# Kernel tuning notes

Measured on AMD Instinct MI355X. Metric: run time of the kernel, lower is better.

## Reference

```python
import jax, jax.numpy as jnp
import numpy as np

B, S, E = 2, 2048, 1024
H = 16
D = E // H          # head dim = 64
K_TOP = 64          # top-k tokens kept per query in sparse branch
M = 256             # performer kernel feature dim
EPS = 1e-6


def setup_inputs() -> dict:
    key = jax.random.key(0)
    ks = jax.random.split(key, 16)
    sc = 0.02
    p = {
        'x': jax.random.normal(ks[0], (B, S, E), jnp.float32),
        # sparse-attention branch params
        'Wq_s': jax.random.normal(ks[1], (E, E), jnp.float32) * sc,
        'Wk_s': jax.random.normal(ks[2], (E, E), jnp.float32) * sc,
        'Wv_s': jax.random.normal(ks[3], (E, E), jnp.float32) * sc,
        'Wo_s': jax.random.normal(ks[4], (E, E), jnp.float32) * sc,
        'bq_s': jnp.zeros((E,), jnp.float32),
        'bk_s': jnp.zeros((E,), jnp.float32),
        'bv_s': jnp.zeros((E,), jnp.float32),
        'bo_s': jnp.zeros((E,), jnp.float32),
        # performer branch params
        'Wq_p': jax.random.normal(ks[5], (E, E), jnp.float32) * sc,
        'Wk_p': jax.random.normal(ks[6], (E, E), jnp.float32) * sc,
        'Wv_p': jax.random.normal(ks[7], (E, E), jnp.float32) * sc,
        'Wo_p': jax.random.normal(ks[8], (E, E), jnp.float32) * sc,
        'bo_p': jnp.zeros((E,), jnp.float32),
        'Wfeat': jax.random.normal(ks[9], (D, M), jnp.float32) / np.sqrt(D),
        # gate
        'Wg': jax.random.normal(ks[10], (E, 2), jnp.float32) * sc,
        'bg': jnp.zeros((2,), jnp.float32),
    }
    return p


def _split_heads(t):
    # [B,S,E] -> [B,H,S,D]
    return t.reshape(B, S, H, D).transpose(0, 2, 1, 3)


def _merge_heads(t):
    # [B,H,S,D] -> [B,S,E]
    return t.transpose(0, 2, 1, 3).reshape(B, S, E)


def _sparse_attn(x, Wq, bq, Wk, bk, Wv, bv, Wo, bo):
    q = _split_heads(x @ Wq + bq)
    k = _split_heads(x @ Wk + bk)
    v = _split_heads(x @ Wv + bv)
    scores = jnp.einsum('bhqd,bhkd->bhqk', q, k) / np.sqrt(D)  # [B,H,S,S]
    # keep only top-K scores per query row
    topv = jax.lax.top_k(scores, K_TOP)[0]
    thresh = topv[..., -1:]
    neg = jnp.finfo(scores.dtype).min
    masked = jnp.where(scores >= thresh, scores, neg)
    attn = jax.nn.softmax(masked, axis=-1)
    out = jnp.einsum('bhqk,bhkd->bhqd', attn, v)
    return _merge_heads(out) @ Wo + bo


def _performer_attn(x, Wq, Wk, Wv, Wo, bo, Wfeat):
    q = _split_heads(x @ Wq)
    k = _split_heads(x @ Wk)
    v = _split_heads(x @ Wv)
    # learned relu feature map (FAVOR-style linear attention)
    phi_q = jax.nn.relu(jnp.einsum('bhsd,dm->bhsm', q, Wfeat)) + EPS
    phi_k = jax.nn.relu(jnp.einsum('bhsd,dm->bhsm', k, Wfeat)) + EPS
    kv = jnp.einsum('bhsm,bhsd->bhmd', phi_k, v)      # [B,H,M,D]
    z = phi_k.sum(axis=2)                              # [B,H,M]
    num = jnp.einsum('bhsm,bhmd->bhsd', phi_q, kv)
    den = jnp.einsum('bhsm,bhm->bhs', phi_q, z)[..., None] + EPS
    return _merge_heads(num / den) @ Wo + bo


def reference(x, Wq_s, Wk_s, Wv_s, Wo_s, bq_s, bk_s, bv_s, bo_s,
              Wq_p, Wk_p, Wv_p, Wo_p, bo_p, Wfeat, Wg, bg):
    sparse_out = _sparse_attn(x, Wq_s, bq_s, Wk_s, bk_s, Wv_s, bv_s, Wo_s, bo_s)
    perf_out = _performer_attn(x, Wq_p, Wk_p, Wv_p, Wo_p, bo_p, Wfeat)
    avg_hidden = x.mean(axis=1)                        # [B,E]
    gate = jax.nn.softmax(avg_hidden @ Wg + bg, axis=-1)  # [B,2]
    w_s = gate[:, 0][:, None, None]
    w_p = gate[:, 1][:, None, None]
    # dropout is identity in eval/reference mode
    return w_s * sparse_out + w_p * perf_out
```

## Files before the change

### kernel.cpp

```cpp
#include <hip/hip_runtime.h>


constexpr int cB = 2, cS = 2048, cE = 1024, cH = 16, cD = 64, cKTOP = 64, cM = 256;
constexpr float cEPS = 1e-6f;

typedef _Float16 half8 __attribute__((ext_vector_type(8)));
typedef float f32x16 __attribute__((ext_vector_type(16)));

__device__ __forceinline__ unsigned int f2key(float f) {
    unsigned int u = __float_as_uint(f);
    return (u & 0x80000000u) ? ~u : (u | 0x80000000u);
}

__device__ __forceinline__ unsigned short h2u(_Float16 h) {
    union { _Float16 h; unsigned short u; } x; x.h = h; return x.u;
}

__device__ __forceinline__ half8 ld_half8(const unsigned short* p) {
    union { uint4 u; half8 h; } x;
    x.u = *(const uint4*)p;
    return x.h;
}

__global__ __launch_bounds__(256)
void gemm_qk_blas(const float* __restrict__ A,
                  const float* __restrict__ W,
                  const float* __restrict__ bias,
                  float* __restrict__ C, int K, int N)
{
    __shared__ __align__(16) float As[16][68];
    __shared__ __align__(16) float Bs[16][68];
    const int t  = threadIdx.x;
    const int r0 = blockIdx.y * 64;
    const int c0 = blockIdx.x * 64;
    const int tm = t >> 4, tn = t & 15;
    float pacc[4][4] = {};
    float cacc[4][4] = {};

    const int ar = t >> 2, ak = (t & 3) * 4;
    const int bk = t >> 4, bc = (t & 15) * 4;

    for (int k0 = 0; k0 < K; k0 += 16) {
        const float4 av = *(const float4*)(A + (size_t)(r0 + ar) * K + (k0 + ak));
        const float4 bv = *(const float4*)(W + (size_t)(k0 + bk) * N + (c0 + bc));
        As[ak + 0][ar] = av.x;
        As[ak + 1][ar] = av.y;
        As[ak + 2][ar] = av.z;
        As[ak + 3][ar] = av.w;
        *(float4*)&Bs[bk][bc] = bv;
        __syncthreads();
        #pragma unroll
        for (int kk = 0; kk < 16; ++kk) {
            const float4 a4 = *(const float4*)&As[kk][tm * 4];
            const float4 b4 = *(const float4*)&Bs[kk][tn * 4];
            const float a[4]  = {a4.x, a4.y, a4.z, a4.w};
            const float bb[4] = {b4.x, b4.y, b4.z, b4.w};
            #pragma unroll
            for (int i = 0; i < 4; ++i)
                #pragma unroll
                for (int j = 0; j < 4; ++j)
                    pacc[i][j] = fmaf(a[i], bb[j], pacc[i][j]);
        }
        __syncthreads();
        const int kn = k0 + 16;
        if (kn == 384 || kn == 768 || kn == K) {
            #pragma unroll
            for (int i = 0; i < 4; ++i)
                #pragma unroll
                for (int j = 0; j < 4; ++j) {
                    cacc[i][j] = cacc[i][j] + pacc[i][j];
                    pacc[i][j] = 0.f;
                }
        }
    }
    #pragma unroll
    for (int i = 0; i < 4; ++i) {
        const int r = r0 + tm * 4 + i;
        const int c = c0 + tn * 4;
        float4 v;
        v.x = cacc[i][0] + bias[c + 0];
        v.y = cacc[i][1] + bias[c + 1];
        v.z = cacc[i][2] + bias[c + 2];
        v.w = cacc[i][3] + bias[c + 3];
        *(float4*)&C[(size_t)r * N + c] = v;
    }
}

__global__ __launch_bounds__(256)
void conv_wT(const float* __restrict__ W,
             unsigned short* __restrict__ wthi,
             unsigned short* __restrict__ wtlo)
{
    __shared__ float tile[64][68];
    const int t  = threadIdx.x;
    const int k0 = blockIdx.y * 64;
    const int n0 = blockIdx.x * 64;
    const int r  = t >> 4, c4 = (t & 15) * 4;
    #pragma unroll
    for (int i = 0; i < 4; ++i) {
        const int k = r + 16 * i;
        const float4 v = *(const float4*)&W[(size_t)(k0 + k) * cE + n0 + c4];
        tile[k][c4 + 0] = v.x; tile[k][c4 + 1] = v.y;
        tile[k][c4 + 2] = v.z; tile[k][c4 + 3] = v.w;
    }
    __syncthreads();
    #pragma unroll
    for (int i = 0; i < 4; ++i) {
        const int n = r + 16 * i;
        unsigned int hp[2], lp[2];
        #pragma unroll
        for (int p = 0; p < 2; ++p) {
            unsigned short hh[2], ll[2];
            #pragma unroll
            for (int j = 0; j < 2; ++j) {
                const float f = tile[c4 + p * 2 + j][n];
                const _Float16 h = (_Float16)f;
                hh[j] = h2u(h);
                ll[j] = h2u((_Float16)(f - (float)h));
            }
            hp[p] = (unsigned int)hh[0] | ((unsigned int)hh[1] << 16);
            lp[p] = (unsigned int)ll[0] | ((unsigned int)ll[1] << 16);
        }
        uint2 hv, lv;
        hv.x = hp[0]; hv.y = hp[1];
        lv.x = lp[0]; lv.y = lp[1];
        *(uint2*)&wthi[(size_t)(n0 + n) * cE + k0 + c4] = hv;
        *(uint2*)&wtlo[(size_t)(n0 + n) * cE + k0 + c4] = lv;
    }
}

__global__ __launch_bounds__(256)
void gemm_hilo(const float* __restrict__ A,
               const unsigned short* __restrict__ wthi,
               const unsigned short* __restrict__ wtlo,
               const float* __restrict__ bias,
               float* __restrict__ C)
{
    __shared__ __align__(16) unsigned short Ah[128][24];
    __shared__ __align__(16) unsigned short Al[128][24];
    __shared__ __align__(16) unsigned short Bh[64][24];
    __shared__ __align__(16) unsigned short Bl[64][24];

    const int t    = threadIdx.x;
    const int lane = t & 63, wave = t >> 6;
    const int wr   = wave >> 1, wc = wave & 1;
    const int r0   = blockIdx.y * 128, c0 = blockIdx.x * 64;
    const int fr   = lane & 31, g5 = lane >> 5;

    const int arow = t >> 1, aka = (t & 1) * 8;
    const int bsel = t >> 7;
    const int brow = (t & 127) >> 1, bkb = (t & 1) * 8;
    const unsigned short* wsrc = bsel ? wtlo : wthi;

    f32x16 acc0 = {0.f,0.f,0.f,0.f,0.f,0.f,0.f,0.f,0.f,0.f,0.f,0.f,0.f,0.f,0.f,0.f};
    f32x16 acc1 = {0.f,0.f,0.f,0.f,0.f,0.f,0.f,0.f,0.f,0.f,0.f,0.f,0.f,0.f,0.f,0.f};

    for (int k0 = 0; k0 < cE; k0 += 16) {
        const float4 x0 = *(const float4*)&A[(size_t)(r0 + arow) * cE + k0 + aka];
        const float4 x1 = *(const float4*)&A[(size_t)(r0 + arow) * cE + k0 + aka + 4];
        const float xf[8] = {x0.x, x0.y, x0.z, x0.w, x1.x, x1.y, x1.z, x1.w};
        unsigned int hw[4], lw[4];
        #pragma unroll
        for (int p = 0; p < 4; ++p) {
            unsigned short hh[2], ll[2];
            #pragma unroll
            for (int j = 0; j < 2; ++j) {
                const float f = xf[p * 2 + j];
                const _Float16 h = (_Float16)f;
                hh[j] = h2u(h);
                ll[j] = h2u((_Float16)(f - (float)h));
            }
            hw[p] = (unsigned int)hh[0] | ((unsigned int)hh[1] << 16);
            lw[p] = (unsigned int)ll[0] | ((unsigned int)ll[1] << 16);
        }
        uint4 hv, lv;
        hv.x = hw[0]; hv.y = hw[1]; hv.z = hw[2]; hv.w = hw[3];
        lv.x = lw[0]; lv.y = lw[1]; lv.z = lw[2]; lv.w = lw[3];
        *(uint4*)&Ah[arow][aka] = hv;
        *(uint4*)&Al[arow][aka] = lv;

        const uint4 wv = *(const uint4*)&wsrc[(size_t)(c0 + brow) * cE + k0 + bkb];
        if (bsel) *(uint4*)&Bl[brow][bkb] = wv;
        else      *(uint4*)&Bh[brow][bkb] = wv;
        __syncthreads();

        const half8 a0h = ld_half8(&Ah[wr * 64 + fr][g5 * 8]);
        const half8 a0l = ld_half8(&Al[wr * 64 + fr][g5 * 8]);
        const half8 a1h = ld_half8(&Ah[wr * 64 + 32 + fr][g5 * 8]);
        const half8 a1l = ld_half8(&Al[wr * 64 + 32 + fr][g5 * 8]);
        const half8 bh  = ld_half8(&Bh[wc * 32 + fr][g5 * 8]);
        const half8 bl  = ld_half8(&Bl[wc * 32 + fr][g5 * 8]);

        acc0 = __builtin_amdgcn_mfma_f32_32x32x16_f16(a0l, bh, acc0, 0, 0, 0);
        acc0 = __builtin_amdgcn_mfma_f32_32x32x16_f16(a0h, bl, acc0, 0, 0, 0);
        acc0 = __builtin_amdgcn_mfma_f32_32x32x16_f16(a0h, bh, acc0, 0, 0, 0);
        acc1 = __builtin_amdgcn_mfma_f32_32x32x16_f16(a1l, bh, acc1, 0, 0, 0);
        acc1 = __builtin_amdgcn_mfma_f32_32x32x16_f16(a1h, bl, acc1, 0, 0, 0);
        acc1 = __builtin_amdgcn_mfma_f32_32x32x16_f16(a1h, bh, acc1, 0, 0, 0);
        __syncthreads();
    }

    const int col = c0 + wc * 32 + fr;
    const float bv = bias ? bias[col] : 0.f;
    #pragma unroll
    for (int rg = 0; rg < 16; ++rg) {
        const int row = r0 + wr * 64 + (rg & 3) + 8 * (rg >> 2) + 4 * g5;
        C[(size_t)row * cE + col] = acc0[rg] + bv;
    }
    #pragma unroll
    for (int rg = 0; rg < 16; ++rg) {
        const int row = r0 + wr * 64 + 32 + (rg & 3) + 8 * (rg >> 2) + 4 * g5;
        C[(size_t)row * cE + col] = acc1[rg] + bv;
    }
}

__global__ __launch_bounds__(256)
void out_gemm_hilo(const float* __restrict__ As_, const float* __restrict__ Ap_,
                   const unsigned short* __restrict__ w1hi,
                   const unsigned short* __restrict__ w1lo,
                   const unsigned short* __restrict__ w2hi,
                   const unsigned short* __restrict__ w2lo,
                   const float* __restrict__ bos, const float* __restrict__ bop,
                   const float* __restrict__ gates, float* __restrict__ out)
{
    __shared__ __align__(16) unsigned short A1h[128][24], A1l[128][24];
    __shared__ __align__(16) unsigned short A2h[128][24], A2l[128][24];
    __shared__ __align__(16) unsigned short B1h[64][24],  B1l[64][24];
    __shared__ __align__(16) unsigned short B2h[64][24],  B2l[64][24];

    const int t    = threadIdx.x;
    const int lane = t & 63, wave = t >> 6;
    const int wr   = wave >> 1, wc = wave & 1;
    const int r0   = blockIdx.y * 128, c0 = blockIdx.x * 64;
    const int fr   = lane & 31, g5 = lane >> 5;
    const int b    = r0 >> 11;
    const float gs = gates[b * 2 + 0], gp = gates[b * 2 + 1];

    const int arow = t >> 1, aka = (t & 1) * 8;
    const int bsel = t >> 7;
    const int brow = (t & 127) >> 1, bkb = (t & 1) * 8;
    const unsigned short* s1 = bsel ? w1lo : w1hi;
    const unsigned short* s2 = bsel ? w2lo : w2hi;

    f32x16 acc0 = {0.f,0.f,0.f,0.f,0.f,0.f,0.f,0.f,0.f,0.f,0.f,0.f,0.f,0.f,0.f,0.f};
    f32x16 acc1 = {0.f,0.f,0.f,0.f,0.f,0.f,0.f,0.f,0.f,0.f,0.f,0.f,0.f,0.f,0.f,0.f};

    for (int k0 = 0; k0 < cE; k0 += 16) {
        {
            const float4 x0 = *(const float4*)&As_[(size_t)(r0 + arow) * cE + k0 + aka];
            const float4 x1 = *(const float4*)&As_[(size_t)(r0 + arow) * cE + k0 + aka + 4];
            const float xf[8] = {x0.x * gs, x0.y * gs, x0.z * gs, x0.w * gs,
                                 x1.x * gs, x1.y * gs, x1.z * gs, x1.w * gs};
            unsigned int hw[4], lw[4];
            #pragma unroll
            for (int p = 0; p < 4; ++p) {
                unsigned short hh[2], ll[2];
                #pragma unroll
                for (int j = 0; j < 2; ++j) {
                    const float f = xf[p * 2 + j];
                    const _Float16 h = (_Float16)f;
                    hh[j] = h2u(h);
                    ll[j] = h2u((_Float16)(f - (float)h));
                }
                hw[p] = (unsigned int)hh[0] | ((unsigned int)hh[1] << 16);
                lw[p] = (unsigned int)ll[0] | ((unsigned int)ll[1] << 16);
            }
            uint4 hv, lv;
            hv.x = hw[0]; hv.y = hw[1]; hv.z = hw[2]; hv.w = hw[3];
            lv.x = lw[0]; lv.y = lw[1]; lv.z = lw[2]; lv.w = lw[3];
            *(uint4*)&A1h[arow][aka] = hv;
            *(uint4*)&A1l[arow][aka] = lv;
        }
        {
            const float4 x0 = *(const float4*)&Ap_[(size_t)(r0 + arow) * cE + k0 + aka];
            const float4 x1 = *(const float4*)&Ap_[(size_t)(r0 + arow) * cE + k0 + aka + 4];
            const float xf[8] = {x0.x * gp, x0.y * gp, x0.z * gp, x0.w * gp,
                                 x1.x * gp, x1.y * gp, x1.z * gp, x1.w * gp};
            unsigned int hw[4], lw[4];
            #pragma unroll
            for (int p = 0; p < 4; ++p) {
                unsigned short hh[2], ll[2];
                #pragma unroll
                for (int j = 0; j < 2; ++j) {
                    const float f = xf[p * 2 + j];
                    const _Float16 h = (_Float16)f;
                    hh[j] = h2u(h);
                    ll[j] = h2u((_Float16)(f - (float)h));
                }
                hw[p] = (unsigned int)hh[0] | ((unsigned int)hh[1] << 16);
                lw[p] = (unsigned int)ll[0] | ((unsigned int)ll[1] << 16);
            }
            uint4 hv, lv;
            hv.x = hw[0]; hv.y = hw[1]; hv.z = hw[2]; hv.w = hw[3];
            lv.x = lw[0]; lv.y = lw[1]; lv.z = lw[2]; lv.w = lw[3];
            *(uint4*)&A2h[arow][aka] = hv;
            *(uint4*)&A2l[arow][aka] = lv;
        }
        {
            const uint4 w1 = *(const uint4*)&s1[(size_t)(c0 + brow) * cE + k0 + bkb];
            if (bsel) *(uint4*)&B1l[brow][bkb] = w1;
            else      *(uint4*)&B1h[brow][bkb] = w1;
            const uint4 w2 = *(const uint4*)&s2[(size_t)(c0 + brow) * cE + k0 + bkb];
            if (bsel) *(uint4*)&B2l[brow][bkb] = w2;
            else      *(uint4*)&B2h[brow][bkb] = w2;
        }
        __syncthreads();

        const half8 b1h = ld_half8(&B1h[wc * 32 + fr][g5 * 8]);
        const half8 b1l = ld_half8(&B1l[wc * 32 + fr][g5 * 8]);
        const half8 b2h = ld_half8(&B2h[wc * 32 + fr][g5 * 8]);
        const half8 b2l = ld_half8(&B2l[wc * 32 + fr][g5 * 8]);
        {
            const half8 a1h = ld_half8(&A1h[wr * 64 + fr][g5 * 8]);
            const half8 a1l = ld_half8(&A1l[wr * 64 + fr][g5 * 8]);
            const half8 a2h = ld_half8(&A2h[wr * 64 + fr][g5 * 8]);
            const half8 a2l = ld_half8(&A2l[wr * 64 + fr][g5 * 8]);
            acc0 = __builtin_amdgcn_mfma_f32_32x32x16_f16(a1l, b1h, acc0, 0, 0, 0);
            acc0 = __builtin_amdgcn_mfma_f32_32x32x16_f16(a1h, b1l, acc0, 0, 0, 0);
            acc0 = __builtin_amdgcn_mfma_f32_32x32x16_f16(a1h, b1h, acc0, 0, 0, 0);
            acc0 = __builtin_amdgcn_mfma_f32_32x32x16_f16(a2l, b2h, acc0, 0, 0, 0);
            acc0 = __builtin_amdgcn_mfma_f32_32x32x16_f16(a2h, b2l, acc0, 0, 0, 0);
            acc0 = __builtin_amdgcn_mfma_f32_32x32x16_f16(a2h, b2h, acc0, 0, 0, 0);
        }
        {
            const half8 a1h = ld_half8(&A1h[wr * 64 + 32 + fr][g5 * 8]);
            const half8 a1l = ld_half8(&A1l[wr * 64 + 32 + fr][g5 * 8]);
            const half8 a2h = ld_half8(&A2h[wr * 64 + 32 + fr][g5 * 8]);
            const half8 a2l = ld_half8(&A2l[wr * 64 + 32 + fr][g5 * 8]);
            acc1 = __builtin_amdgcn_mfma_f32_32x32x16_f16(a1l, b1h, acc1, 0, 0, 0);
            acc1 = __builtin_amdgcn_mfma_f32_32x32x16_f16(a1h, b1l, acc1, 0, 0, 0);
            acc1 = __builtin_amdgcn_mfma_f32_32x32x16_f16(a1h, b1h, acc1, 0, 0, 0);
            acc1 = __builtin_amdgcn_mfma_f32_32x32x16_f16(a2l, b2h, acc1, 0, 0, 0);
            acc1 = __builtin_amdgcn_mfma_f32_32x32x16_f16(a2h, b2l, acc1, 0, 0, 0);
            acc1 = __builtin_amdgcn_mfma_f32_32x32x16_f16(a2h, b2h, acc1, 0, 0, 0);
        }
        __syncthreads();
    }

    const int col = c0 + wc * 32 + fr;
    const float bv = gs * bos[col] + gp * bop[col];
    #pragma unroll
    for (int rg = 0; rg < 16; ++rg) {
        const int row = r0 + wr * 64 + (rg & 3) + 8 * (rg >> 2) + 4 * g5;
        out[(size_t)row * cE + col] = acc0[rg] + bv;
    }
    #pragma unroll
    for (int rg = 0; rg < 16; ++rg) {
        const int row = r0 + wr * 64 + 32 + (rg & 3) + 8 * (rg >> 2) + 4 * g5;
        out[(size_t)row * cE + col] = acc1[rg] + bv;
    }
}

__global__ __launch_bounds__(256)
void transpose_k(const float* __restrict__ Ks, float* __restrict__ KsT)
{
    __shared__ float tile[64][65];
    const int t  = threadIdx.x;
    const int bh = blockIdx.y;
    const int b  = bh >> 4;
    const int h64 = (bh & 15) * 64;
    const int s0 = blockIdx.x * 64;
    const int sr = t >> 4;
    const int d4 = (t & 15) * 4;
    #pragma unroll
    for (int i = 0; i < 4; ++i) {
        const int s = sr + 16 * i;
        float4 v = *(const float4*)&Ks[((size_t)(b * cS + s0 + s)) * cE + h64 + d4];
        tile[s][d4 + 0] = v.x; tile[s][d4 + 1] = v.y;
        tile[s][d4 + 2] = v.z; tile[s][d4 + 3] = v.w;
    }
    __syncthreads();
    const int s4 = (t & 15) * 4;
    #pragma unroll
    for (int i = 0; i < 4; ++i) {
        const int d = (t >> 4) + 16 * i;
        float4 w;
        w.x = tile[s4 + 0][d]; w.y = tile[s4 + 1][d];
        w.z = tile[s4 + 2][d]; w.w = tile[s4 + 3][d];
        *(float4*)&KsT[((size_t)(bh * 64 + d)) * cS + s0 + s4] = w;
    }
}

__global__ __launch_bounds__(256, 4)
void sparse_attn(const float* __restrict__ Q, const float* __restrict__ KT,
                 const float* __restrict__ Ks, const float* __restrict__ V,
                 float* __restrict__ O)
{
    __shared__ float QfT[64][8];
    __shared__ unsigned int hist[8][257];
    __shared__ unsigned int hist2[8][257];
    __shared__ unsigned short cidx[8][128];
    __shared__ double cval[8][128];
    __shared__ float cw[8][128];
    __shared__ int cnt[8];
    __shared__ int t16hi[8], rem[8], t16[8];
    __shared__ double T64s[8], s65s[8], rowm[8];

    const int t   = threadIdx.x;
    const int bh  = blockIdx.y;
    const int b   = bh >> 4;
    const int h64 = (bh & 15) * 64;
    const int q0  = blockIdx.x * 8;

    if (t < 128) {
        const int r = t >> 4, c4 = (t & 15) * 4;
        const float4 v =
            *(const float4*)&Q[((size_t)(b * cS + q0 + r)) * cE + h64 + c4];
        QfT[c4 + 0][r] = v.x; QfT[c4 + 1][r] = v.y;
        QfT[c4 + 2][r] = v.z; QfT[c4 + 3][r] = v.w;
    }
    for (int i = t; i < 8 * 257; i += 256) {
        (&hist[0][0])[i]  = 0u;
        (&hist2[0][0])[i] = 0u;
    }
    if (t < 8) cnt[t] = 0;
    __syncthreads();

    const float* KTh = KT + (size_t)bh * 64 * cS;
    float4 acc[2][8];
    #pragma unroll
    for (int j = 0; j < 2; ++j)
        #pragma unroll
        for (int r = 0; r < 8; ++r) acc[j][r] = make_float4(0.f, 0.f, 0.f, 0.f);

    #pragma unroll 4
    for (int d = 0; d < 64; ++d) {
        const float4 k0 = *(const float4*)&KTh[(size_t)d * cS + 4 * t];
        const float4 k1 = *(const float4*)&KTh[(size_t)d * cS + 1024 + 4 * t];
        const float4 qa = *(const float4*)&QfT[d][0];
        const float4 qb = *(const float4*)&QfT[d][4];
        const float qr[8] = {qa.x, qa.y, qa.z, qa.w, qb.x, qb.y, qb.z, qb.w};
        #pragma unroll
        for (int r = 0; r < 8; ++r) {
            acc[0][r].x = fmaf(qr[r], k0.x, acc[0][r].x);
            acc[0][r].y = fmaf(qr[r], k0.y, acc[0][r].y);
            acc[0][r].z = fmaf(qr[r], k0.z, acc[0][r].z);
            acc[0][r].w = fmaf(qr[r], k0.w, acc[0][r].w);
            acc[1][r].x = fmaf(qr[r], k1.x, acc[1][r].x);
            acc[1][r].y = fmaf(qr[r], k1.y, acc[1][r].y);
            acc[1][r].z = fmaf(qr[r], k1.z, acc[1][r].z);
            acc[1][r].w = fmaf(qr[r], k1.w, acc[1][r].w);
        }
    }
    unsigned int su[2][8][2];
    #pragma unroll
    for (int j = 0; j < 2; ++j)
        #pragma unroll
        for (int r = 0; r < 8; ++r) {
            su[j][r][0] = (f2key(acc[j][r].x * 0.125f) >> 16)
                        | ((f2key(acc[j][r].y * 0.125f) >> 16) << 16);
            su[j][r][1] = (f2key(acc[j][r].z * 0.125f) >> 16)
                        | ((f2key(acc[j][r].w * 0.125f) >> 16) << 16);
        }

    #pragma unroll
    for (int j = 0; j < 2; ++j)
        #pragma unroll
        for (int r = 0; r < 8; ++r)
            #pragma unroll
            for (int w = 0; w < 2; ++w) {
                const unsigned int u = su[j][r][w];
                atomicAdd(&hist[r][(u & 0xFFFFu) >> 8], 1u);
                atomicAdd(&hist[r][u >> 24], 1u);
            }
    __syncthreads();
    if (t < 8) {
        int need = cKTOP + 1;
        int hb = 0;
        for (int bin = 255; bin >= 0; --bin) {
            const int c = (int)hist[t][bin];
            if (c >= need) { hb = bin; break; }
            need -= c;
        }
        t16hi[t] = hb;
        rem[t] = need;
    }
    __syncthreads();
    #pragma unroll
    for (int j = 0; j < 2; ++j)
        #pragma unroll
        for (int r = 0; r < 8; ++r) {
            const unsigned int hb = (unsigned int)t16hi[r];
            #pragma unroll
            for (int w = 0; w < 2; ++w) {
                const unsigned int u  = su[j][r][w];
                const unsigned int lo = u & 0xFFFFu;
                const unsigned int hi = u >> 16;
                if ((lo >> 8) == hb) atomicAdd(&hist2[r][lo & 255u], 1u);
                if ((hi >> 8) == hb) atomicAdd(&hist2[r][hi & 255u], 1u);
            }
        }
    __syncthreads();
    if (t < 8) {
        int need = rem[t];
        int lb = 0;
        for (int bin = 255; bin >= 0; --bin) {
            const int c = (int)hist2[t][bin];
            if (c >= need) { lb = bin; break; }
            need -= c;
        }
        t16[t] = (t16hi[t] << 8) | lb;
    }
    __syncthreads();

    #pragma unroll
    for (int j = 0; j < 2; ++j)
        #pragma unroll
        for (int r = 0; r < 8; ++r) {
            const int thr16 = max(t16[r] - 2, 0);
            #pragma unroll
            for (int w = 0; w < 2; ++w) {
                const unsigned int u = su[j][r][w];
                const int v0 = (int)(u & 0xFFFFu);
                const int v1 = (int)(u >> 16);
                if (v0 >= thr16) {
                    const int slot = atomicAdd(&cnt[r], 1);
                    if (slot < 128)
                        cidx[r][slot] = (unsigned short)(j * 1024 + 4 * t + w * 2);
                }
                if (v1 >= thr16) {
                    const int slot = atomicAdd(&cnt[r], 1);
                    if (slot < 128)
                        cidx[r][slot] = (unsigned short)(j * 1024 + 4 * t + w * 2 + 1);
                }
            }
        }
    __syncthreads();

    const int wv = t >> 6, lane = t & 63;
    #pragma unroll
    for (int rx = 0; rx < 2; ++rx) {
        const int rr = wv * 2 + rx;
        const int n = min(cnt[rr], 128);
        for (int c = lane; c < n; c += 64) {
            const int key = cidx[rr][c];
            const float* kp = Ks + ((size_t)(b * cS + key)) * cE + h64;
            double a = 0.0;
            #pragma unroll 4
            for (int d4 = 0; d4 < 64; d4 += 4) {
                const float4 kv = *(const float4*)&kp[d4];
                a = fma((double)QfT[d4 + 0][rr], (double)kv.x, a);
                a = fma((double)QfT[d4 + 1][rr], (double)kv.y, a);
                a = fma((double)QfT[d4 + 2][rr], (double)kv.z, a);
                a = fma((double)QfT[d4 + 3][rr], (double)kv.w, a);
            }
            cval[rr][c] = a * 0.125;
        }
    }
    __syncthreads();

    #pragma unroll
    for (int rx = 0; rx < 2; ++rx) {
        const int rr = wv * 2 + rx;
        const int n = min(cnt[rr], 128);
        for (int c = lane; c < n; c += 64) {
            const double v = cval[rr][c];
            int rank = 0;
            for (int i = 0; i < n; ++i) rank += (cval[rr][i] > v) ? 1 : 0;
            if (rank == 0)  rowm[rr] = v;
            if (rank == 63) T64s[rr] = v;
            if (rank == 64) s65s[rr] = v;
        }
    }
    __syncthreads();

    #pragma unroll
    for (int rx = 0; rx < 2; ++rx) {
        const int rr = wv * 2 + rx;
        const int n = min(cnt[rr], 128);
        const double T64 = T64s[rr], s65 = s65s[rr], m = rowm[rr];
        float za = 0.f;
        for (int c = lane; c < n; c += 64) {
            const double v = cval[rr][c];
            if (v >= T64) za += expf((float)(v - m));
        }
        #pragma unroll
        for (int off = 32; off >= 1; off >>= 1)
            za += __shfl_xor(za, off);
        const float g   = (float)(T64 - s65);
        const float gm  = fmaxf(g - 5e-7f, 0.f);
        const float wB  = 0.5f * erfcf(gm * (1.0f / 2.2e-6f));
        const float wA  = 1.f - wB;
        const float e64 = expf((float)(T64 - m));
        const float e65 = expf((float)(s65 - m));
        const float ZB  = za - e64 + e65;
        const float cIn = wA / za + wB / ZB;
        const float c64 = wA / za;
        const float c65 = wB / ZB;
        for (int c = lane; c < n; c += 64) {
            const double v = cval[rr][c];
            float cc = 0.f;
            if (v > T64)       cc = cIn;
            else if (v == T64) cc = c64;
            else if (v == s65) cc = c65;
            cw[rr][c] = (cc != 0.f) ? cc * expf((float)(v - m)) : 0.f;
        }
    }
    __syncthreads();

    #pragma unroll
    for (int rx = 0; rx < 2; ++rx) {
        const int rr = wv * 2 + rx;
        const int n = min(cnt[rr], 128);
        float o = 0.f;
        int j = 0;
        for (; j + 8 <= n; j += 8) {
            float wreg[8];
            int   kreg[8];
            #pragma unroll
            for (int u = 0; u < 8; ++u) {
                wreg[u] = cw[rr][j + u];
                kreg[u] = cidx[rr][j + u];
            }
            float vreg[8];
            #pragma unroll
            for (int u = 0; u < 8; ++u)
                vreg[u] = V[((size_t)(b * cS + kreg[u])) * cE + h64 + lane];
            #pragma unroll
            for (int u = 0; u < 8; ++u)
                o = fmaf(wreg[u], vreg[u], o);
        }
        for (; j < n; ++j)
            o = fmaf(cw[rr][j],
                     V[((size_t)(b * cS + cidx[rr][j])) * cE + h64 + lane], o);
        O[((size_t)(b * cS + q0 + rr)) * cE + h64 + lane] = o;
    }
}

__global__ __launch_bounds__(256)
void perf_kv(const float* __restrict__ Kp, const float* __restrict__ Vp,
             const float* __restrict__ Wfeat,
             float* __restrict__ kvpart, float* __restrict__ zpart)
{
    __shared__ __align__(16) float Wf[64][68];
    __shared__ __align__(16) float Kt[64][68];
    __shared__ __align__(16) float Vt[64][68];
    __shared__ __align__(16) float Ph[64][68];
    const int t    = threadIdx.x;
    const int mc   = blockIdx.x & 3;
    const int sc   = blockIdx.x >> 2;
    const int bh   = blockIdx.y;
    const int b    = bh >> 4;
    const int h64  = (bh & 15) * 64;
    const int m0   = mc * 64;
    const int sbase = sc * 1024;

    #pragma unroll
    for (int i = 0; i < 4; ++i) {
        const int lin = t + 256 * i;
        const int d   = lin >> 4;
        const int m4  = (lin & 15) * 4;
        *(float4*)&Wf[d][m4] = *(const float4*)&Wfeat[d * cM + m0 + m4];
    }

    const int tm = t >> 4, tn = t & 15;
    const int sr = tm * 4;
    const int cn = tn * 4;
    float akv[4][4] = {};
    float az = 0.f;

    for (int st = 0; st < 16; ++st) {
        const int s0g = sbase + st * 64;
        __syncthreads();
        #pragma unroll
        for (int i = 0; i < 4; ++i) {
            const int row = tm + 16 * i;
            const size_t base = ((size_t)(b * cS + s0g + row)) * cE + h64 + cn;
            *(float4*)&Kt[row][cn] = *(const float4*)&Kp[base];
            *(float4*)&Vt[row][cn] = *(const float4*)&Vp[base];
        }
        __syncthreads();
        float4 p0 = {0,0,0,0}, p1 = {0,0,0,0}, p2 = {0,0,0,0}, p3 = {0,0,0,0};
        #pragma unroll 8
        for (int d = 0; d < 64; ++d) {
            const float4 wv = *(const float4*)&Wf[d][cn];
            const float k0 = Kt[sr + 0][d], k1 = Kt[sr + 1][d];
            const float k2 = Kt[sr + 2][d], k3 = Kt[sr + 3][d];
            p0.x = fmaf(k0, wv.x, p0.x); p0.y = fmaf(k0, wv.y, p0.y);
            p0.z = fmaf(k0, wv.z, p0.z); p0.w = fmaf(k0, wv.w, p0.w);
            p1.x = fmaf(k1, wv.x, p1.x); p1.y = fmaf(k1, wv.y, p1.y);
            p1.z = fmaf(k1, wv.z, p1.z); p1.w = fmaf(k1, wv.w, p1.w);
            p2.x = fmaf(k2, wv.x, p2.x); p2.y = fmaf(k2, wv.y, p2.y);
// ... 96 lines not shown
        if (t < 64)
            zl[t] = zpart[(size_t)bh * cM + m0 + t] + zpart[(size_t)(32 + bh) * cM + m0 + t];
        __syncthreads();
        float4 p0 = {0,0,0,0}, p1 = {0,0,0,0}, p2 = {0,0,0,0}, p3 = {0,0,0,0};
        #pragma unroll 8
        for (int d = 0; d < 64; ++d) {
            const float4 wv = *(const float4*)&Wf[d][cn];
            const float q0 = Qt[sr + 0][d], q1 = Qt[sr + 1][d];
            const float q2 = Qt[sr + 2][d], q3 = Qt[sr + 3][d];
            p0.x = fmaf(q0, wv.x, p0.x); p0.y = fmaf(q0, wv.y, p0.y);
            p0.z = fmaf(q0, wv.z, p0.z); p0.w = fmaf(q0, wv.w, p0.w);
            p1.x = fmaf(q1, wv.x, p1.x); p1.y = fmaf(q1, wv.y, p1.y);
            p1.z = fmaf(q1, wv.z, p1.z); p1.w = fmaf(q1, wv.w, p1.w);
            p2.x = fmaf(q2, wv.x, p2.x); p2.y = fmaf(q2, wv.y, p2.y);
            p2.z = fmaf(q2, wv.z, p2.z); p2.w = fmaf(q2, wv.w, p2.w);
            p3.x = fmaf(q3, wv.x, p3.x); p3.y = fmaf(q3, wv.y, p3.y);
            p3.z = fmaf(q3, wv.z, p3.z); p3.w = fmaf(q3, wv.w, p3.w);
        }
        p0.x = fmaxf(p0.x, 0.f) + cEPS; p0.y = fmaxf(p0.y, 0.f) + cEPS;
        p0.z = fmaxf(p0.z, 0.f) + cEPS; p0.w = fmaxf(p0.w, 0.f) + cEPS;
        p1.x = fmaxf(p1.x, 0.f) + cEPS; p1.y = fmaxf(p1.y, 0.f) + cEPS;
        p1.z = fmaxf(p1.z, 0.f) + cEPS; p1.w = fmaxf(p1.w, 0.f) + cEPS;
        p2.x = fmaxf(p2.x, 0.f) + cEPS; p2.y = fmaxf(p2.y, 0.f) + cEPS;
        p2.z = fmaxf(p2.z, 0.f) + cEPS; p2.w = fmaxf(p2.w, 0.f) + cEPS;
        p3.x = fmaxf(p3.x, 0.f) + cEPS; p3.y = fmaxf(p3.y, 0.f) + cEPS;
        p3.z = fmaxf(p3.z, 0.f) + cEPS; p3.w = fmaxf(p3.w, 0.f) + cEPS;
        *(float4*)&Ph[sr + 0][cn] = p0;
        *(float4*)&Ph[sr + 1][cn] = p1;
        *(float4*)&Ph[sr + 2][cn] = p2;
        *(float4*)&Ph[sr + 3][cn] = p3;
        __syncthreads();
        #pragma unroll 8
        for (int mm = 0; mm < 64; ++mm) {
            const float4 kvv = *(const float4*)&KV[mm][cn];
            const float a0 = Ph[sr + 0][mm], a1 = Ph[sr + 1][mm];
            const float a2 = Ph[sr + 2][mm], a3 = Ph[sr + 3][mm];
            num[0][0] = fmaf(a0, kvv.x, num[0][0]); num[0][1] = fmaf(a0, kvv.y, num[0][1]);
            num[0][2] = fmaf(a0, kvv.z, num[0][2]); num[0][3] = fmaf(a0, kvv.w, num[0][3]);
            num[1][0] = fmaf(a1, kvv.x, num[1][0]); num[1][1] = fmaf(a1, kvv.y, num[1][1]);
            num[1][2] = fmaf(a1, kvv.z, num[1][2]); num[1][3] = fmaf(a1, kvv.w, num[1][3]);
            num[2][0] = fmaf(a2, kvv.x, num[2][0]); num[2][1] = fmaf(a2, kvv.y, num[2][1]);
            num[2][2] = fmaf(a2, kvv.z, num[2][2]); num[2][3] = fmaf(a2, kvv.w, num[2][3]);
            num[3][0] = fmaf(a3, kvv.x, num[3][0]); num[3][1] = fmaf(a3, kvv.y, num[3][1]);
            num[3][2] = fmaf(a3, kvv.z, num[3][2]); num[3][3] = fmaf(a3, kvv.w, num[3][3]);
        }
        if (t < 64) {
            float a = 0.f;
            #pragma unroll
            for (int m4 = 0; m4 < 64; m4 += 4) {
                const float4 ph = *(const float4*)&Ph[t][m4];
                const float4 zz = *(const float4*)&zl[m4];
                a = fmaf(ph.x, zz.x, a); a = fmaf(ph.y, zz.y, a);
                a = fmaf(ph.z, zz.z, a); a = fmaf(ph.w, zz.w, a);
            }
            dacc += a;
        }
    }
    __syncthreads();
    if (t < 64) den[t] = dacc + cEPS;
    __syncthreads();
    #pragma unroll
    for (int i = 0; i < 4; ++i) {
        const float di = 1.f / den[sr + i];
        float4 v;
        v.x = num[i][0] * di; v.y = num[i][1] * di;
        v.z = num[i][2] * di; v.w = num[i][3] * di;
        *(float4*)&Ap[((size_t)(b * cS + s0 + sr + i)) * cE + h64 + cn] = v;
    }
}

__global__ __launch_bounds__(256)
void gate_avg(const float* __restrict__ x, double* __restrict__ avgpart)
{
    const int i  = blockIdx.x * 256 + threadIdx.x;
    const int sc = blockIdx.y;
    const int b  = i >> 10, e = i & 1023;
    double acc = 0.0;
    const int sEnd = sc * 128 + 128;
    for (int s = sc * 128; s < sEnd; ++s)
        acc += (double)x[((size_t)(b * cS + s)) * cE + e];
    avgpart[(size_t)sc * 2048 + i] = acc;
}

__global__ void gate_final(const double* __restrict__ avgpart, const float* __restrict__ Wg,
                           const float* __restrict__ bg, float* __restrict__ gates)
{
    const int t = threadIdx.x;
    const int b = t >> 6, lane = t & 63;
    float l0 = 0.f, l1 = 0.f;
    for (int e = lane; e < cE; e += 64) {
        double s = 0.0;
        #pragma unroll
        for (int sc = 0; sc < 16; ++sc)
            s += avgpart[(size_t)sc * 2048 + b * 1024 + e];
        const float a = (float)(s / (double)cS);
        l0 = fmaf(a, Wg[e * 2 + 0], l0);
        l1 = fmaf(a, Wg[e * 2 + 1], l1);
    }
    for (int off = 32; off >= 1; off >>= 1) {
        l0 += __shfl_down(l0, off);
        l1 += __shfl_down(l1, off);
    }
    if (lane == 0) {
        l0 += bg[0]; l1 += bg[1];
        const float m = fmaxf(l0, l1);
        const float e0 = expf(l0 - m), e1 = expf(l1 - m);
        const float s = e0 + e1;
        gates[b * 2 + 0] = e0 / s;
        gates[b * 2 + 1] = e1 / s;
    }
}

extern "C" void kernel_launch(void* const* d_in, const int* in_sizes, int n_in,
                              void* d_out, int out_size, void* d_ws, size_t ws_size,
                              hipStream_t stream)
{
    (void)in_sizes; (void)n_in; (void)out_size; (void)ws_size;
    const float* x     = (const float*)d_in[0];
    const float* Wq_s  = (const float*)d_in[1];
    const float* Wk_s  = (const float*)d_in[2];
    const float* Wv_s  = (const float*)d_in[3];
    const float* Wo_s  = (const float*)d_in[4];
    const float* bq_s  = (const float*)d_in[5];
    const float* bk_s  = (const float*)d_in[6];
    const float* bv_s  = (const float*)d_in[7];
    const float* bo_s  = (const float*)d_in[8];
    const float* Wq_p  = (const float*)d_in[9];
    const float* Wk_p  = (const float*)d_in[10];
    const float* Wv_p  = (const float*)d_in[11];
    const float* Wo_p  = (const float*)d_in[12];
    const float* bo_p  = (const float*)d_in[13];
    const float* Wfeat = (const float*)d_in[14];
    const float* Wg    = (const float*)d_in[15];
    const float* bg    = (const float*)d_in[16];

    float* ws = (float*)d_ws;
    const size_t NRE = (size_t)cB * cS * cE;
    float* Qs    = ws;
    float* Ks    = Qs + NRE;
    float* KsT   = Ks + NRE;
    float* Vs    = KsT + NRE;
    float* Asout = Vs + NRE;
    float* kvpart = Asout + NRE;
    float* zpart  = kvpart + (size_t)2 * 32 * cM * cD;
    double* avgpart = (double*)(zpart + (size_t)2 * 32 * cM);
    float* gates = (float*)(avgpart + (size_t)16 * 2048);
    unsigned short* wthi  = (unsigned short*)(gates + 16);
    unsigned short* wtlo  = wthi + (size_t)cE * cE;
    unsigned short* wo1hi = wtlo + (size_t)cE * cE;
    unsigned short* wo1lo = wo1hi + (size_t)cE * cE;
    unsigned short* wo2hi = wo1lo + (size_t)cE * cE;
    unsigned short* wo2lo = wo2hi + (size_t)cE * cE;

    conv_wT<<<dim3(16, 16), 256, 0, stream>>>(Wo_s, wo1hi, wo1lo);
    conv_wT<<<dim3(16, 16), 256, 0, stream>>>(Wo_p, wo2hi, wo2lo);

    gemm_qk_blas<<<dim3(16, 64), 256, 0, stream>>>(x, Wq_s, bq_s, Qs, cE, cE);
    gemm_qk_blas<<<dim3(16, 64), 256, 0, stream>>>(x, Wk_s, bk_s, Ks, cE, cE);
    conv_wT<<<dim3(16, 16), 256, 0, stream>>>(Wv_s, wthi, wtlo);
    gemm_hilo<<<dim3(16, 32), 256, 0, stream>>>(x, wthi, wtlo, bv_s, Vs);
    transpose_k<<<dim3(32, 32), 256, 0, stream>>>(Ks, KsT);
    sparse_attn<<<dim3(256, 32), 256, 0, stream>>>(Qs, KsT, Ks, Vs, Asout);

    float* Qp    = Qs;
    float* Kp    = Ks;
    float* Vp    = Vs;
    float* Apout = KsT;
    conv_wT<<<dim3(16, 16), 256, 0, stream>>>(Wq_p, wthi, wtlo);
    gemm_hilo<<<dim3(16, 32), 256, 0, stream>>>(x, wthi, wtlo, nullptr, Qp);
    conv_wT<<<dim3(16, 16), 256, 0, stream>>>(Wk_p, wthi, wtlo);
    gemm_hilo<<<dim3(16, 32), 256, 0, stream>>>(x, wthi, wtlo, nullptr, Kp);
    conv_wT<<<dim3(16, 16), 256, 0, stream>>>(Wv_p, wthi, wtlo);
    gemm_hilo<<<dim3(16, 32), 256, 0, stream>>>(x, wthi, wtlo, nullptr, Vp);
    perf_kv<<<dim3(8, 32), 256, 0, stream>>>(Kp, Vp, Wfeat, kvpart, zpart);
    perf_numden<<<dim3(32, 32), 256, 0, stream>>>(Qp, Wfeat, kvpart, zpart, Apout);

    gate_avg<<<dim3(8, 16), 256, 0, stream>>>(x, avgpart);
    gate_final<<<dim3(1), 128, 0, stream>>>(avgpart, Wg, bg, gates);
    out_gemm_hilo<<<dim3(16, 32), 256, 0, stream>>>(Asout, Apout,
                                                    wo1hi, wo1lo, wo2hi, wo2lo,
                                                    bo_s, bo_p, gates,
                                                    (float*)d_out);
}
```

Before: 1.572 ms.

## Replace atomic radix-histogram threshold search with wave-reduced binary search

Finds the per-row 16-bit top-k threshold key with a 16-step binary search instead of two 256-bin LDS histograms built with atomics. Each step counts elements at or above the midpoint per thread, reduces the counts with wave shuffles, and combines the four wave partials through a small double-buffered shared array. This removes the histogram zeroing, the contended LDS atomics and the serial single-thread bin scans. In exchange it adds 16 block barriers and 16×8 shuffle reductions per block.

```diff
diff --git a/kernel.cpp b/kernel.cpp
--- a/kernel.cpp
+++ b/kernel.cpp
@@ -387,13 +387,11 @@
                  float* __restrict__ O)
 {
     __shared__ float QfT[64][8];
-    __shared__ unsigned int hist[8][257];
-    __shared__ unsigned int hist2[8][257];
+    __shared__ int wcnt[2][4][8];
     __shared__ unsigned short cidx[8][128];
     __shared__ double cval[8][128];
     __shared__ float cw[8][128];
     __shared__ int cnt[8];
-    __shared__ int t16hi[8], rem[8], t16[8];
     __shared__ double T64s[8], s65s[8], rowm[8];
 
     const int t   = threadIdx.x;
@@ -409,12 +407,10 @@
         QfT[c4 + 0][r] = v.x; QfT[c4 + 1][r] = v.y;
         QfT[c4 + 2][r] = v.z; QfT[c4 + 3][r] = v.w;
     }
-    for (int i = t; i < 8 * 257; i += 256) {
-        (&hist[0][0])[i]  = 0u;
-        (&hist2[0][0])[i] = 0u;
-    }
     if (t < 8) cnt[t] = 0;
     __syncthreads();
+
+    const int wv = t >> 6, lane = t & 63;
 
     const float* KTh = KT + (size_t)bh * 64 * cS;
     float4 acc[2][8];
@@ -453,61 +449,43 @@
                         | ((f2key(acc[j][r].w * 0.125f) >> 16) << 16);
         }
 
+    int lo[8], hi[8];
+    #pragma unroll
+    for (int r = 0; r < 8; ++r) { lo[r] = 0; hi[r] = 65536; }
+
+    for (int it = 0; it < 16; ++it) {
+        #pragma unroll
+        for (int r = 0; r < 8; ++r) {
+            const int mid = (lo[r] + hi[r]) >> 1;
+            int c = 0;
+            #pragma unroll
+            for (int j = 0; j < 2; ++j)
+                #pragma unroll
+                for (int w = 0; w < 2; ++w) {
+                    const unsigned int u = su[j][r][w];
+                    c += ((int)(u & 0xFFFFu) >= mid) ? 1 : 0;
+                    c += ((int)(u >> 16)     >= mid) ? 1 : 0;
+                }
+            #pragma unroll
+            for (int off = 32; off >= 1; off >>= 1)
+                c += __shfl_xor(c, off);
+            if (lane == 0) wcnt[it & 1][wv][r] = c;
+        }
+        __syncthreads();
+        #pragma unroll
+        for (int r = 0; r < 8; ++r) {
+            const int mid = (lo[r] + hi[r]) >> 1;
+            const int tot = wcnt[it & 1][0][r] + wcnt[it & 1][1][r]
+                          + wcnt[it & 1][2][r] + wcnt[it & 1][3][r];
+            if (tot >= cKTOP + 1) lo[r] = mid; else hi[r] = mid;
+        }
+    }
+
     #pragma unroll
     for (int j = 0; j < 2; ++j)
         #pragma unroll
-        for (int r = 0; r < 8; ++r)
-            #pragma unroll
-            for (int w = 0; w < 2; ++w) {
-                const unsigned int u = su[j][r][w];
-                atomicAdd(&hist[r][(u & 0xFFFFu) >> 8], 1u);
-                atomicAdd(&hist[r][u >> 24], 1u);
-            }
-    __syncthreads();
-    if (t < 8) {
-        int need = cKTOP + 1;
-        int hb = 0;
-        for (int bin = 255; bin >= 0; --bin) {
-            const int c = (int)hist[t][bin];
-            if (c >= need) { hb = bin; break; }
-            need -= c;
-        }
-        t16hi[t] = hb;
-        rem[t] = need;
-    }
-    __syncthreads();
-    #pragma unroll
-    for (int j = 0; j < 2; ++j)
-        #pragma unroll
         for (int r = 0; r < 8; ++r) {
-            const unsigned int hb = (unsigned int)t16hi[r];
-            #pragma unroll
-            for (int w = 0; w < 2; ++w) {
-                const unsigned int u  = su[j][r][w];
-                const unsigned int lo = u & 0xFFFFu;
-                const unsigned int hi = u >> 16;
-                if ((lo >> 8) == hb) atomicAdd(&hist2[r][lo & 255u], 1u);
-                if ((hi >> 8) == hb) atomicAdd(&hist2[r][hi & 255u], 1u);
-            }
-        }
-    __syncthreads();
-    if (t < 8) {
-        int need = rem[t];
-        int lb = 0;
-        for (int bin = 255; bin >= 0; --bin) {
-            const int c = (int)hist2[t][bin];
-            if (c >= need) { lb = bin; break; }
-            need -= c;
-        }
-        t16[t] = (t16hi[t] << 8) | lb;
-    }
-    __syncthreads();
-
-    #pragma unroll
-    for (int j = 0; j < 2; ++j)
-        #pragma unroll
-        for (int r = 0; r < 8; ++r) {
-            const int thr16 = max(t16[r] - 2, 0);
+            const int thr16 = max(lo[r] - 2, 0);
             #pragma unroll
             for (int w = 0; w < 2; ++w) {
                 const unsigned int u = su[j][r][w];
@@ -527,7 +505,6 @@
         }
     __syncthreads();
 
-    const int wv = t >> 6, lane = t & 63;
     #pragma unroll
     for (int rx = 0; rx < 2; ++rx) {
         const int rr = wv * 2 + rx;
```

Measured after the change: 1.606 ms. 2.2% more time.

## Use fp16 MFMA for sparse top-k candidate scoring and drop K transpose

Applied to the files above, without the earlier changes.

The K projection GEMM now also writes an fp16 copy of K, and the sparse attention kernel computes the approximate score matrix with 32x32x16 fp16 MFMA instructions instead of fp32 FMAs over a transposed K. This removes the transpose_k kernel and the fp32 scalar score loop, and reuses one histogram buffer for both radix passes to cut shared memory. The candidate threshold margin is widened from 2 to 3 bins to absorb fp16 rounding error. Exact scores are still recomputed in double for the selected candidates, but the lower precision risks missing a true top-k key or overflowing the 128-slot candidate buffer.

```diff
diff --git a/kernel.cpp b/kernel.cpp
--- a/kernel.cpp
+++ b/kernel.cpp
@@ -26,7 +26,9 @@
 void gemm_qk_blas(const float* __restrict__ A,
                   const float* __restrict__ W,
                   const float* __restrict__ bias,
-                  float* __restrict__ C, int K, int N)
+                  float* __restrict__ C,
+                  unsigned short* __restrict__ khi,
+                  int K, int N)
 {
     __shared__ __align__(16) float As[16][68];
     __shared__ __align__(16) float Bs[16][68];
@@ -83,6 +85,14 @@
         v.z = cacc[i][2] + bias[c + 2];
         v.w = cacc[i][3] + bias[c + 3];
         *(float4*)&C[(size_t)r * N + c] = v;
+        if (khi) {
+            ushort4 hs;
+            hs.x = h2u((_Float16)v.x);
+            hs.y = h2u((_Float16)v.y);
+            hs.z = h2u((_Float16)v.z);
+            hs.w = h2u((_Float16)v.w);
+            *(ushort4*)&khi[(size_t)r * N + c] = hs;
+        }
     }
 }
 
@@ -351,44 +361,15 @@
     }
 }
 
-__global__ __launch_bounds__(256)
-void transpose_k(const float* __restrict__ Ks, float* __restrict__ KsT)
-{
-    __shared__ float tile[64][65];
-    const int t  = threadIdx.x;
-    const int bh = blockIdx.y;
-    const int b  = bh >> 4;
-    const int h64 = (bh & 15) * 64;
-    const int s0 = blockIdx.x * 64;
-    const int sr = t >> 4;
-    const int d4 = (t & 15) * 4;
-    #pragma unroll
-    for (int i = 0; i < 4; ++i) {
-        const int s = sr + 16 * i;
-        float4 v = *(const float4*)&Ks[((size_t)(b * cS + s0 + s)) * cE + h64 + d4];
-        tile[s][d4 + 0] = v.x; tile[s][d4 + 1] = v.y;
-        tile[s][d4 + 2] = v.z; tile[s][d4 + 3] = v.w;
-    }
-    __syncthreads();
-    const int s4 = (t & 15) * 4;
-    #pragma unroll
-    for (int i = 0; i < 4; ++i) {
-        const int d = (t >> 4) + 16 * i;
-        float4 w;
-        w.x = tile[s4 + 0][d]; w.y = tile[s4 + 1][d];
-        w.z = tile[s4 + 2][d]; w.w = tile[s4 + 3][d];
-        *(float4*)&KsT[((size_t)(bh * 64 + d)) * cS + s0 + s4] = w;
-    }
-}
-
 __global__ __launch_bounds__(256, 4)
-void sparse_attn(const float* __restrict__ Q, const float* __restrict__ KT,
+void sparse_attn(const float* __restrict__ Q,
+                 const unsigned short* __restrict__ Khi,
                  const float* __restrict__ Ks, const float* __restrict__ V,
                  float* __restrict__ O)
 {
     __shared__ float QfT[64][8];
+    __shared__ __align__(16) unsigned short Qhi[8][72];
     __shared__ unsigned int hist[8][257];
-    __shared__ unsigned int hist2[8][257];
     __shared__ unsigned short cidx[8][128];
     __shared__ double cval[8][128];
     __shared__ float cw[8][128];
@@ -406,63 +387,55 @@
         const int r = t >> 4, c4 = (t & 15) * 4;
         const float4 v =
             *(const float4*)&Q[((size_t)(b * cS + q0 + r)) * cE + h64 + c4];
-        QfT[c4 + 0][r] = v.x; QfT[c4 + 1][r] = v.y;
-        QfT[c4 + 2][r] = v.z; QfT[c4 + 3][r] = v.w;
-    }
-    for (int i = t; i < 8 * 257; i += 256) {
-        (&hist[0][0])[i]  = 0u;
-        (&hist2[0][0])[i] = 0u;
-    }
+        const float f[4] = {v.x, v.y, v.z, v.w};
+        #pragma unroll
+        for (int i = 0; i < 4; ++i) {
+            QfT[c4 + i][r] = f[i];
+            Qhi[r][c4 + i] = h2u((_Float16)f[i]);
+        }
+    }
+    for (int i = t; i < 8 * 257; i += 256) (&hist[0][0])[i] = 0u;
     if (t < 8) cnt[t] = 0;
     __syncthreads();
 
-    const float* KTh = KT + (size_t)bh * 64 * cS;
-    float4 acc[2][8];
-    #pragma unroll
-    for (int j = 0; j < 2; ++j)
-        #pragma unroll
-        for (int r = 0; r < 8; ++r) acc[j][r] = make_float4(0.f, 0.f, 0.f, 0.f);
-
-    #pragma unroll 4
-    for (int d = 0; d < 64; ++d) {
-        const float4 k0 = *(const float4*)&KTh[(size_t)d * cS + 4 * t];
-        const float4 k1 = *(const float4*)&KTh[(size_t)d * cS + 1024 + 4 * t];
-        const float4 qa = *(const float4*)&QfT[d][0];
-        const float4 qb = *(const float4*)&QfT[d][4];
-        const float qr[8] = {qa.x, qa.y, qa.z, qa.w, qb.x, qb.y, qb.z, qb.w};
-        #pragma unroll
-        for (int r = 0; r < 8; ++r) {
-            acc[0][r].x = fmaf(qr[r], k0.x, acc[0][r].x);
-            acc[0][r].y = fmaf(qr[r], k0.y, acc[0][r].y);
-            acc[0][r].z = fmaf(qr[r], k0.z, acc[0][r].z);
-            acc[0][r].w = fmaf(qr[r], k0.w, acc[0][r].w);
-            acc[1][r].x = fmaf(qr[r], k1.x, acc[1][r].x);
-            acc[1][r].y = fmaf(qr[r], k1.y, acc[1][r].y);
-            acc[1][r].z = fmaf(qr[r], k1.z, acc[1][r].z);
-            acc[1][r].w = fmaf(qr[r], k1.w, acc[1][r].w);
-        }
-    }
-    unsigned int su[2][8][2];
-    #pragma unroll
-    for (int j = 0; j < 2; ++j)
-        #pragma unroll
-        for (int r = 0; r < 8; ++r) {
-            su[j][r][0] = (f2key(acc[j][r].x * 0.125f) >> 16)
-                        | ((f2key(acc[j][r].y * 0.125f) >> 16) << 16);
-            su[j][r][1] = (f2key(acc[j][r].z * 0.125f) >> 16)
-                        | ((f2key(acc[j][r].w * 0.125f) >> 16) << 16);
-        }
-
-    #pragma unroll
-    for (int j = 0; j < 2; ++j)
-        #pragma unroll
-        for (int r = 0; r < 8; ++r)
-            #pragma unroll
-            for (int w = 0; w < 2; ++w) {
-                const unsigned int u = su[j][r][w];
-                atomicAdd(&hist[r][(u & 0xFFFFu) >> 8], 1u);
-                atomicAdd(&hist[r][u >> 24], 1u);
+    const int lane = t & 63;
+    const int wv   = t >> 6;
+    const int col  = lane & 31;
+    const int g5   = lane >> 5;
+    const int r0   = g5 * 4;
+
+    half8 ahi[4];
+    {
+        const int arow = col & 7;
+        #pragma unroll
+        for (int ks = 0; ks < 4; ++ks)
+            ahi[ks] = ld_half8(&Qhi[arow][g5 * 8 + ks * 16]);
+    }
+    unsigned int su[16][2];
+    {
+        const size_t kbase = ((size_t)(b * cS + wv * 512 + col)) * cE + h64;
+        #pragma unroll
+        for (int tl = 0; tl < 16; ++tl) {
+            const unsigned short* kh = Khi + kbase + (size_t)tl * 32 * cE;
+            f32x16 acc = {0.f,0.f,0.f,0.f,0.f,0.f,0.f,0.f,
+                          0.f,0.f,0.f,0.f,0.f,0.f,0.f,0.f};
+            #pragma unroll
+            for (int ks = 0; ks < 4; ++ks) {
+                const half8 bh8 = ld_half8(kh + g5 * 8 + ks * 16);
+                acc = __builtin_amdgcn_mfma_f32_32x32x16_f16(ahi[ks], bh8, acc, 0, 0, 0);
             }
+            const unsigned int k0 = f2key(acc[0] * 0.125f) >> 16;
+            const unsigned int k1 = f2key(acc[1] * 0.125f) >> 16;
+            const unsigned int k2 = f2key(acc[2] * 0.125f) >> 16;
+            const unsigned int k3 = f2key(acc[3] * 0.125f) >> 16;
+            su[tl][0] = k0 | (k1 << 16);
+            su[tl][1] = k2 | (k3 << 16);
+            atomicAdd(&hist[r0 + 0][k0 >> 8], 1u);
+            atomicAdd(&hist[r0 + 1][k1 >> 8], 1u);
+            atomicAdd(&hist[r0 + 2][k2 >> 8], 1u);
+            atomicAdd(&hist[r0 + 3][k3 >> 8], 1u);
+        }
+    }
     __syncthreads();
     if (t < 8) {
         int need = cKTOP + 1;
@@ -476,26 +449,25 @@
         rem[t] = need;
     }
     __syncthreads();
-    #pragma unroll
-    for (int j = 0; j < 2; ++j)
-        #pragma unroll
-        for (int r = 0; r < 8; ++r) {
-            const unsigned int hb = (unsigned int)t16hi[r];
-            #pragma unroll
-            for (int w = 0; w < 2; ++w) {
-                const unsigned int u  = su[j][r][w];
-                const unsigned int lo = u & 0xFFFFu;
-                const unsigned int hi = u >> 16;
-                if ((lo >> 8) == hb) atomicAdd(&hist2[r][lo & 255u], 1u);
-                if ((hi >> 8) == hb) atomicAdd(&hist2[r][hi & 255u], 1u);
-            }
+    for (int i = t; i < 8 * 257; i += 256) (&hist[0][0])[i] = 0u;
+    __syncthreads();
+    #pragma unroll
+    for (int tl = 0; tl < 16; ++tl)
+        #pragma unroll
+        for (int w = 0; w < 2; ++w) {
+            const unsigned int u = su[tl][w];
+            const int rlo = r0 + 2 * w, rhi = rlo + 1;
+            const unsigned int vlo = u & 0xFFFFu;
+            const unsigned int vhi = u >> 16;
+            if ((int)(vlo >> 8) == t16hi[rlo]) atomicAdd(&hist[rlo][vlo & 255u], 1u);
+            if ((int)(vhi >> 8) == t16hi[rhi]) atomicAdd(&hist[rhi][vhi & 255u], 1u);
         }
     __syncthreads();
     if (t < 8) {
         int need = rem[t];
         int lb = 0;
         for (int bin = 255; bin >= 0; --bin) {
-            const int c = (int)hist2[t][bin];
+            const int c = (int)hist[t][bin];
             if (c >= need) { lb = bin; break; }
             need -= c;
         }
@@ -504,30 +476,26 @@
     __syncthreads();
 
     #pragma unroll
-    for (int j = 0; j < 2; ++j)
-        #pragma unroll
-        for (int r = 0; r < 8; ++r) {
-            const int thr16 = max(t16[r] - 2, 0);
-            #pragma unroll
-            for (int w = 0; w < 2; ++w) {
-                const unsigned int u = su[j][r][w];
-                const int v0 = (int)(u & 0xFFFFu);
-                const int v1 = (int)(u >> 16);
-                if (v0 >= thr16) {
-                    const int slot = atomicAdd(&cnt[r], 1);
-                    if (slot < 128)
-                        cidx[r][slot] = (unsigned short)(j * 1024 + 4 * t + w * 2);
-                }
-                if (v1 >= thr16) {
-                    const int slot = atomicAdd(&cnt[r], 1);
-                    if (slot < 128)
-                        cidx[r][slot] = (unsigned short)(j * 1024 + 4 * t + w * 2 + 1);
-                }
+    for (int tl = 0; tl < 16; ++tl) {
+        const int key = wv * 512 + tl * 32 + col;
+        #pragma unroll
+        for (int w = 0; w < 2; ++w) {
+            const unsigned int u = su[tl][w];
+            const int rlo = r0 + 2 * w, rhi = rlo + 1;
+            const int v0 = (int)(u & 0xFFFFu);
+            const int v1 = (int)(u >> 16);
+            if (v0 >= max(t16[rlo] - 3, 0)) {
+                const int slot = atomicAdd(&cnt[rlo], 1);
+                if (slot < 128) cidx[rlo][slot] = (unsigned short)key;
             }
-        }
-    __syncthreads();
-
-    const int wv = t >> 6, lane = t & 63;
+            if (v1 >= max(t16[rhi] - 3, 0)) {
+                const int slot = atomicAdd(&cnt[rhi], 1);
+                if (slot < 128) cidx[rhi][slot] = (unsigned short)key;
+            }
+        }
+    }
+    __syncthreads();
+
     #pragma unroll
     for (int rx = 0; rx < 2; ++rx) {
         const int rr = wv * 2 + rx;
@@ -930,15 +898,18 @@
     unsigned short* wo2hi = wo1lo + (size_t)cE * cE;
     unsigned short* wo2lo = wo2hi + (size_t)cE * cE;
 
+    unsigned short* Khi = (unsigned short*)KsT;
+
     conv_wT<<<dim3(16, 16), 256, 0, stream>>>(Wo_s, wo1hi, wo1lo);
     conv_wT<<<dim3(16, 16), 256, 0, stream>>>(Wo_p, wo2hi, wo2lo);
 
-    gemm_qk_blas<<<dim3(16, 64), 256, 0, stream>>>(x, Wq_s, bq_s, Qs, cE, cE);
-    gemm_qk_blas<<<dim3(16, 64), 256, 0, stream>>>(x, Wk_s, bk_s, Ks, cE, cE);
+    gemm_qk_blas<<<dim3(16, 64), 256, 0, stream>>>(x, Wq_s, bq_s, Qs,
+                                                   nullptr, cE, cE);
+    gemm_qk_blas<<<dim3(16, 64), 256, 0, stream>>>(x, Wk_s, bk_s, Ks,
+                                                   Khi, cE, cE);
     conv_wT<<<dim3(16, 16), 256, 0, stream>>>(Wv_s, wthi, wtlo);
     gemm_hilo<<<dim3(16, 32), 256, 0, stream>>>(x, wthi, wtlo, bv_s, Vs);
-    transpose_k<<<dim3(32, 32), 256, 0, stream>>>(Ks, KsT);
-    sparse_attn<<<dim3(256, 32), 256, 0, stream>>>(Qs, KsT, Ks, Vs, Asout);
+    sparse_attn<<<dim3(256, 32), 256, 0, stream>>>(Qs, Khi, Ks, Vs, Asout);
 
     float* Qp    = Qs;
     float* Kp    = Ks;
```

Result: faster. 1.434 ms (-8.8%).
